# Performance work log

Hardware: AMD Instinct MI355X
Metric: run time of the kernel (lower is better)

Reference implementation:

```python
import jax, jax.numpy as jnp
import numpy as np

N, E, F_IN, D, B = 20000, 50000, 16, 64, 128


def setup_inputs() -> dict:
    key = jax.random.key(0)
    ks = jax.random.split(key, 24)
    s = 0.05
    inp = {
        "x": jax.random.normal(ks[0], (N, F_IN), jnp.float32),
        "edge_index": jax.random.randint(ks[1], (2, E), 0, N, jnp.int32),
        "edge_attr": jax.random.uniform(ks[2], (E, 5), jnp.float32),
        "batch": jnp.sort(jax.random.randint(ks[3], (N,), 0, B, jnp.int32)),
        # lin0
        "lin0_w": jax.random.normal(ks[4], (D, F_IN)) * s,
        "lin0_b": jnp.zeros((D,), jnp.float32),
        # edge MLP: Linear(5,128) -> ReLU -> Linear(128, D*D)
        "mlp_w1": jax.random.normal(ks[5], (128, 5)) * s,
        "mlp_b1": jnp.zeros((128,), jnp.float32),
        "mlp_w2": jax.random.normal(ks[6], (D * D, 128)) * s,
        "mlp_b2": jnp.zeros((D * D,), jnp.float32),
        # NNConv bias (root_weight=False, bias=True)
        "conv_b": jnp.zeros((D,), jnp.float32),
        # GRU(dim, dim), single layer
        "gru_w_ih": jax.random.normal(ks[7], (3 * D, D)) * s,
        "gru_w_hh": jax.random.normal(ks[8], (3 * D, D)) * s,
        "gru_b_ih": jnp.zeros((3 * D,), jnp.float32),
        "gru_b_hh": jnp.zeros((3 * D,), jnp.float32),
        # Set2Set LSTM(2*dim, dim)
        "lstm_w_ih": jax.random.normal(ks[9], (4 * D, 2 * D)) * s,
        "lstm_w_hh": jax.random.normal(ks[10], (4 * D, D)) * s,
        "lstm_b_ih": jnp.zeros((4 * D,), jnp.float32),
        "lstm_b_hh": jnp.zeros((4 * D,), jnp.float32),
    }
    return inp


def _gru_cell(x, h, w_ih, w_hh, b_ih, b_hh):
    gi = x @ w_ih.T + b_ih
    gh = h @ w_hh.T + b_hh
    i_r, i_z, i_n = jnp.split(gi, 3, axis=-1)
    h_r, h_z, h_n = jnp.split(gh, 3, axis=-1)
    r = jax.nn.sigmoid(i_r + h_r)
    z = jax.nn.sigmoid(i_z + h_z)
    n = jnp.tanh(i_n + r * h_n)
    return (1.0 - z) * n + z * h


def _lstm_cell(x, h, c, w_ih, w_hh, b_ih, b_hh):
    g = x @ w_ih.T + b_ih + h @ w_hh.T + b_hh
    i, f, gg, o = jnp.split(g, 4, axis=-1)
    c_new = jax.nn.sigmoid(f) * c + jax.nn.sigmoid(i) * jnp.tanh(gg)
    h_new = jax.nn.sigmoid(o) * jnp.tanh(c_new)
    return h_new, c_new


def reference(x, edge_index, edge_attr, batch,
              lin0_w, lin0_b, mlp_w1, mlp_b1, mlp_w2, mlp_b2, conv_b,
              gru_w_ih, gru_w_hh, gru_b_ih, gru_b_hh,
              lstm_w_ih, lstm_w_hh, lstm_b_ih, lstm_b_hh):
    src, dst = edge_index[0], edge_index[1]

    out = jax.nn.relu(x @ lin0_w.T + lin0_b)  # [N, D]
    h = out  # GRU hidden (seq_len=1 -> out == h after each step)

    # Edge-conditioned weights: MLP(edge_attr) -> [E, D, D]
    hidden = jax.nn.relu(edge_attr @ mlp_w1.T + mlp_b1)
    W_e = (hidden @ mlp_w2.T + mlp_b2).reshape(E, D, D)

    # in-degree counts for mean aggregation
    deg = jax.ops.segment_sum(jnp.ones((E,), x.dtype), dst, num_segments=N)
    deg = jnp.maximum(deg, 1.0)[:, None]

    for _ in range(3):
        # NNConv: gather src feats, per-edge matmul, scatter-mean to dst
        msg = jnp.einsum('ed,edo->eo', out[src], W_e)  # [E, D]
        agg = jax.ops.segment_sum(msg, dst, num_segments=N) / deg
        m = jax.nn.relu(agg + conv_b)
        h = _gru_cell(m, h, gru_w_ih, gru_w_hh, gru_b_ih, gru_b_hh)
        out = h

    # Set2Set pooling, 3 processing steps
    q_star = jnp.zeros((B, 2 * D), x.dtype)
    hh = jnp.zeros((B, D), x.dtype)
    cc = jnp.zeros((B, D), x.dtype)
    for _ in range(3):
        hh, cc = _lstm_cell(q_star, hh, cc, lstm_w_ih, lstm_w_hh, lstm_b_ih, lstm_b_hh)
        q = hh  # [B, D]
        e = jnp.sum(out * q[batch], axis=-1)  # [N]
        e_max = jax.ops.segment_max(e, batch, num_segments=B)
        a = jnp.exp(e - e_max[batch])
        a = a / jax.ops.segment_sum(a, batch, num_segments=B)[batch]
        r = jax.ops.segment_sum(a[:, None] * out, batch, num_segments=B)  # [B, D]
        q_star = jnp.concatenate([q, r], axis=-1)

    return q_star  # [B, 2*D]
```

## Files before the change

### kernel.cpp

```cpp
#include <hip/hip_runtime.h>
#include <hip/hip_bf16.h>

typedef float BF;
__device__ __forceinline__ float ldf(const BF* p, int i) { return p[i]; }

typedef _Float16 h8 __attribute__((ext_vector_type(8)));
typedef float f4 __attribute__((ext_vector_type(4)));

static constexpr int N_NODES = 20000;
static constexpr int N_EDGES = 50000;
static constexpr int E_PAD   = 50176;
static constexpr int N_MSGB  = 392;
static constexpr int N_PAD   = 20032;
static constexpr int BROW    = 136;
static constexpr int SROW    = 72;
static constexpr int N_B     = 79;
static constexpr int MAXSEG  = 2048;

__device__ __forceinline__ float sigf(float x) { return 1.f / (1.f + __expf(-x)); }
__device__ __forceinline__ float tanh_f(float x) {
  float e = __expf(2.f * x);
  return 1.f - 2.f / (e + 1.f);
}

static constexpr int S1_LIN0 = 5000;
static constexpr int S1_QS   = 2048;
static constexpr int S1_WCAT = 128;
static constexpr int S1_B2S  = 16;
static constexpr int S1_DEG  = 196;
static constexpr int PREP1_BLOCKS = S1_LIN0 + S1_QS + S1_WCAT + S1_B2S + 1 + 1 + S1_DEG;

__global__ void k_prep1(const BF* __restrict__ x, const int* __restrict__ batch,
                        const int* __restrict__ dst,
                        const BF* __restrict__ w0, const BF* __restrict__ b0,
                        const BF* __restrict__ w2, const BF* __restrict__ b2,
                        const BF* __restrict__ gwih, const BF* __restrict__ gwhh,
                        const BF* __restrict__ gbih, const BF* __restrict__ gbhh,
                        float* __restrict__ h, _Float16* __restrict__ h16,
                        _Float16* __restrict__ Qs, _Float16* __restrict__ Wcat,
                        float* __restrict__ bcat, _Float16* __restrict__ b2s,
                        int* __restrict__ seg, int* __restrict__ degi,
                        int* __restrict__ bsum) {
  int bid = blockIdx.x, t = threadIdx.x;
  if (bid < S1_LIN0) {
    __shared__ float xs[64];
    if (t < 64) xs[t] = ldf(x, bid * 64 + t);
    __syncthreads();
    int nl = t >> 6, o = t & 63;
    float acc = ldf(b0, o);
#pragma unroll
    for (int f = 0; f < 16; ++f) acc += xs[nl * 16 + f] * ldf(w0, o * 16 + f);
    float v = fmaxf(acc, 0.f);
    int idx = bid * 256 + t;
    h[idx] = v;
    h16[idx] = (_Float16)v;
    return;
  }
  bid -= S1_LIN0;
  if (bid < S1_QS) {
    int i = bid * 256 + t;
    int dl = i >> 13, rem = i & 8191;
    int f = rem >> 9, ln = (rem >> 3) & 63, j = i & 7;
    int o = (f & 3) * 16 + (ln & 15);
    int k = (f >> 2) * 32 + (ln >> 4) * 8 + j;
    Qs[i] = (_Float16)ldf(w2, (dl * 64 + o) * 128 + k);
    return;
  }
  bid -= S1_QS;
  if (bid < S1_WCAT) {
    int idx = bid * 256 + t, row = idx >> 7, k = idx & 127;
    int g = row >> 6, rr = row & 63;
    float v = 0.f;
    if (g == 0) v = (k < 64) ? ldf(gwih, rr * 64 + k) : ldf(gwhh, rr * 64 + (k - 64));
    else if (g == 1) v = (k < 64) ? ldf(gwih, (64 + rr) * 64 + k) : ldf(gwhh, (64 + rr) * 64 + (k - 64));
    else if (g == 2) v = (k < 64) ? ldf(gwih, (128 + rr) * 64 + k) : 0.f;
    else v = (k < 64) ? 0.f : ldf(gwhh, (128 + rr) * 64 + (k - 64));
    Wcat[idx] = (_Float16)v;
    return;
  }
  bid -= S1_WCAT;
  if (bid < S1_B2S) {
    int idx = bid * 256 + t;
    int f = idx >> 9, ln = (idx >> 3) & 63, j = idx & 7;
    int o = (f & 3) * 16 + (ln & 15);
    int d = (f >> 2) * 32 + (ln >> 4) * 8 + j;
    b2s[idx] = (_Float16)ldf(b2, d * 64 + o);
    return;
  }
  bid -= S1_B2S;
  if (bid == 0) {
    float v;
    if (t < 128) v = ldf(gbih, t) + ldf(gbhh, t);
    else if (t < 192) v = ldf(gbih, t);
    else v = ldf(gbhh, t - 64);
    bcat[t] = v;
    return;
  }
  bid -= 1;
  if (bid == 0) {
    if (t > 128) return;
    if (t == 128) { seg[128] = N_NODES; return; }
    int lo = 0, hi = N_NODES;
    while (lo < hi) {
      int mid = (lo + hi) >> 1;
      if (batch[mid] < t) lo = mid + 1; else hi = mid;
    }
    seg[t] = lo;
    return;
  }
  bid -= 1;
  {
    int e = bid * 256 + t;
    if (e < N_EDGES) {
      int d = dst[e];
      atomicAdd(&degi[d], 1);
      atomicAdd(&bsum[d >> 8], 1);
    }
  }
}

__global__ void k_scanA(const int* __restrict__ bsum, int* __restrict__ boff) {
  __shared__ int sd[128];
  int t = threadIdx.x;
  int x = (t < N_B) ? bsum[t] : 0;
  sd[t] = x;
  __syncthreads();
#pragma unroll
  for (int o = 1; o < 128; o <<= 1) {
    int val = (t >= o) ? sd[t - o] : 0;
    __syncthreads();
    sd[t] += val;
    __syncthreads();
  }
  if (t < N_B) boff[t] = sd[t] - x;
}

__global__ void k_scanB(const int* __restrict__ degi, const int* __restrict__ boff,
                        int* __restrict__ cursor) {
  __shared__ int sd[256];
  int b = blockIdx.x, t = threadIdx.x;
  int v = b * 256 + t;
  int x = (v < N_NODES) ? degi[v] : 0;
  sd[t] = x;
  __syncthreads();
#pragma unroll
  for (int o = 1; o < 256; o <<= 1) {
    int val = (t >= o) ? sd[t - o] : 0;
    __syncthreads();
    sd[t] += val;
    __syncthreads();
  }
  if (v < N_NODES) cursor[v] = boff[b] + sd[t] - x;
}

__global__ void k_fill(const int* __restrict__ dst, int* __restrict__ cursor,
                       int* __restrict__ eperm) {
  int e = blockIdx.x * 256 + threadIdx.x;
  if (e < N_EDGES) {
    int pos = atomicAdd(&cursor[dst[e]], 1);
    eperm[pos] = e;
  }
}

static constexpr int S2_MLP = E_PAD / 2;
static constexpr int S2_SP  = 196;

__global__ void k_prep2(const BF* __restrict__ ea, const int* __restrict__ src,
                        const int* __restrict__ dst, const int* __restrict__ eperm,
                        const BF* __restrict__ w1, const BF* __restrict__ b1,
                        _Float16* __restrict__ hidf, int* __restrict__ spadp,
                        int* __restrict__ dpadp) {
  int bid = blockIdx.x, t = threadIdx.x;
  if (bid < S2_MLP) {
    __shared__ float eas[10];
    __shared__ int el2[2];
    if (t < 2) { int pos = bid * 2 + t; el2[t] = (pos < N_EDGES) ? eperm[pos] : -1; }
    __syncthreads();
    if (t < 10) { int e = el2[t / 5]; eas[t] = (e >= 0) ? ldf(ea, e * 5 + (t % 5)) : 0.f; }
    __syncthreads();
    int le = t >> 7, j = t & 127;
    int pos = bid * 2 + le;
    float v = 0.f;
    if (pos < N_EDGES) {
      float acc = ldf(b1, j);
#pragma unroll
      for (int i = 0; i < 5; ++i) acc += eas[le * 5 + i] * ldf(w1, j * 5 + i);
      v = fmaxf(acc, 0.f);
    }
    hidf[(size_t)pos * 128 + j] = (_Float16)v;
    return;
  }
  bid -= S2_MLP;
  {
    int pos = bid * 256 + t;
    if (pos < E_PAD) {
      int e = (pos < N_EDGES) ? eperm[pos] : -1;
      spadp[pos] = (e >= 0) ? src[e] : 0;
      dpadp[pos] = (e >= 0) ? dst[e] : 0;
    }
  }
}

__launch_bounds__(256, 2)
__global__ void k_msg(const _Float16* __restrict__ h16, const _Float16* __restrict__ hidf,
                      const _Float16* __restrict__ Qs, const _Float16* __restrict__ b2s,
                      const int* __restrict__ spadp, const int* __restrict__ dpadp,
                      float* __restrict__ agg) {
  __shared__ _Float16 s_lds[128 * SROW];
  __shared__ _Float16 b_lds[2][8192];
  __shared__ _Float16 b2l[4096];
  const int tid = threadIdx.x;
  const int wv = tid >> 6, ln = tid & 63;
  const int m0 = ln & 15, quad = ln >> 4;
  const int tb = blockIdx.x * 128;

  {
    int el = tid >> 1, half = (tid & 1) * 32;
    int sp_ = spadp[tb + el];
    const uint4* hp4 = (const uint4*)(h16 + (size_t)sp_ * 64 + half);
    uint4 a0 = hp4[0], a1 = hp4[1], a2 = hp4[2], a3 = hp4[3];
    *(uint4*)&s_lds[el * SROW + half] = a0;
    *(uint4*)&s_lds[el * SROW + half + 8] = a1;
    *(uint4*)&s_lds[el * SROW + half + 16] = a2;
    *(uint4*)&s_lds[el * SROW + half + 24] = a3;
  }
  {
    const uint4* sp4 = (const uint4*)b2s;
    *(uint4*)&b2l[tid * 16] = sp4[tid * 2];
    *(uint4*)&b2l[tid * 16 + 8] = sp4[tid * 2 + 1];
  }
  h8 hvv[2][4];
#pragma unroll
  for (int mt = 0; mt < 2; ++mt) {
    int e = tb + wv * 32 + mt * 16 + m0;
    const _Float16* hp = hidf + (size_t)e * 128 + quad * 8;
#pragma unroll
    for (int c = 0; c < 4; ++c) hvv[mt][c] = *(const h8*)(hp + c * 32);
  }
  uint4 breg[4];
  {
    const uint4* qb = (const uint4*)Qs;
#pragma unroll
    for (int c = 0; c < 4; ++c) breg[c] = qb[tid + c * 256];
#pragma unroll
    for (int c = 0; c < 4; ++c) *(uint4*)&b_lds[0][(tid + c * 256) * 8] = breg[c];
  }
  __syncthreads();

  f4 acc[2][4];
#pragma unroll
  for (int mt = 0; mt < 2; ++mt)
#pragma unroll
    for (int ct = 0; ct < 4; ++ct)
#pragma unroll
      for (int j = 0; j < 4; ++j) acc[mt][ct][j] = 0.f;

  for (int dl = 0; dl < 64; ++dl) {
    int cur = dl & 1;
    if (dl < 63) {
      const uint4* qb = (const uint4*)(Qs + (size_t)(dl + 1) * 8192);
#pragma unroll
      for (int c = 0; c < 4; ++c) breg[c] = qb[tid + c * 256];
    }
    _Float16 sv0 = s_lds[(wv * 32 + m0) * SROW + dl];
    _Float16 sv1 = s_lds[(wv * 32 + 16 + m0) * SROW + dl];
#pragma unroll
    for (int t = 0; t < 4; ++t) {
      h8 a0 = hvv[0][t] * sv0;
      h8 a1 = hvv[1][t] * sv1;
#pragma unroll
      for (int ct = 0; ct < 4; ++ct) {
        h8 b = *(const h8*)&b_lds[cur][(t * 4 + ct) * 512 + ln * 8];
        acc[0][ct] = __builtin_amdgcn_mfma_f32_16x16x32_f16(a0, b, acc[0][ct], 0, 0, 0);
        acc[1][ct] = __builtin_amdgcn_mfma_f32_16x16x32_f16(a1, b, acc[1][ct], 0, 0, 0);
      }
    }
    if (dl < 63) {
#pragma unroll
      for (int c = 0; c < 4; ++c) *(uint4*)&b_lds[cur ^ 1][(tid + c * 256) * 8] = breg[c];
    }
    __syncthreads();
  }
#pragma unroll
  for (int tp = 0; tp < 2; ++tp) {
    h8 a0 = *(const h8*)&s_lds[(wv * 32 + m0) * SROW + tp * 32 + quad * 8];
    h8 a1 = *(const h8*)&s_lds[(wv * 32 + 16 + m0) * SROW + tp * 32 + quad * 8];
#pragma unroll
    for (int ct = 0; ct < 4; ++ct) {
      h8 b = *(const h8*)&b2l[(tp * 4 + ct) * 512 + ln * 8];
      acc[0][ct] = __builtin_amdgcn_mfma_f32_16x16x32_f16(a0, b, acc[0][ct], 0, 0, 0);
      acc[1][ct] = __builtin_amdgcn_mfma_f32_16x16x32_f16(a1, b, acc[1][ct], 0, 0, 0);
    }
  }
#pragma unroll
  for (int mt = 0; mt < 2; ++mt) {
#pragma unroll
    for (int r = 0; r < 4; ++r) {
      int pos = tb + wv * 32 + mt * 16 + quad * 4 + r;
      if (pos < N_EDGES) {
        float* ap = agg + (size_t)dpadp[pos] * 64 + m0;
#pragma unroll
        for (int ct = 0; ct < 4; ++ct) atomicAdd(ap + ct * 16, acc[mt][ct][r]);
      }
    }
  }
}

__launch_bounds__(256)
__global__ void k_gru(float* __restrict__ agg, const int* __restrict__ degi,
                      const BF* __restrict__ convb, const _Float16* __restrict__ W,
                      const float* __restrict__ bcat, float* __restrict__ h,
                      _Float16* __restrict__ h16) {
  __shared__ _Float16 xa[64 * BROW];
  __shared__ _Float16 wb[256 * BROW];
  __shared__ float bsh[256];
  int tid = threadIdx.x;
  int wv = tid >> 6, ln = tid & 63, m0 = ln & 15, quad = ln >> 4;
  int rowblk = blockIdx.x * 64;
  bsh[tid] = bcat[tid];
  {
    int r = tid >> 2, c0 = (tid & 3) * 16;
    int node = rowblk + r;
    _Float16 mv[16], hv[16];
    if (node < N_NODES) {
      float inv = 1.f / (float)max(degi[node], 1);
      float* ap = agg + (size_t)node * 64 + c0;
      const float* hp = h + (size_t)node * 64 + c0;
#pragma unroll
      for (int i = 0; i < 16; i += 4) {
        float4 a = *(float4*)(ap + i);
        *(float4*)(ap + i) = make_float4(0.f, 0.f, 0.f, 0.f);
        float4 hf = *(const float4*)(hp + i);
        mv[i + 0] = (_Float16)fmaxf(a.x * inv + ldf(convb, c0 + i + 0), 0.f);
        mv[i + 1] = (_Float16)fmaxf(a.y * inv + ldf(convb, c0 + i + 1), 0.f);
        mv[i + 2] = (_Float16)fmaxf(a.z * inv + ldf(convb, c0 + i + 2), 0.f);
        mv[i + 3] = (_Float16)fmaxf(a.w * inv + ldf(convb, c0 + i + 3), 0.f);
        hv[i + 0] = (_Float16)hf.x; hv[i + 1] = (_Float16)hf.y;
        hv[i + 2] = (_Float16)hf.z; hv[i + 3] = (_Float16)hf.w;
      }
    } else {
#pragma unroll
      for (int i = 0; i < 16; ++i) { mv[i] = (_Float16)0.f; hv[i] = (_Float16)0.f; }
    }
    *(uint4*)&xa[r * BROW + c0] = *(const uint4*)&mv[0];
    *(uint4*)&xa[r * BROW + c0 + 8] = *(const uint4*)&mv[8];
    *(uint4*)&xa[r * BROW + 64 + c0] = *(const uint4*)&hv[0];
    *(uint4*)&xa[r * BROW + 64 + c0 + 8] = *(const uint4*)&hv[8];
  }
#pragma unroll
  for (int c = 0; c < 16; ++c) {
    int i = tid + c * 256, r = i >> 4, ch = i & 15;
    *(uint4*)&wb[r * BROW + ch * 8] = *(const uint4*)(W + (size_t)r * 128 + ch * 8);
  }
  __syncthreads();
  f4 acc[16];
#pragma unroll
  for (int ct = 0; ct < 16; ++ct)
#pragma unroll
    for (int j = 0; j < 4; ++j) acc[ct][j] = 0.f;
#pragma unroll
  for (int t = 0; t < 4; ++t) {
    h8 a = *(const h8*)&xa[(wv * 16 + m0) * BROW + t * 32 + quad * 8];
#pragma unroll
    for (int ct = 0; ct < 16; ++ct) {
      h8 b = *(const h8*)&wb[(ct * 16 + m0) * BROW + t * 32 + quad * 8];
      acc[ct] = __builtin_amdgcn_mfma_f32_16x16x32_f16(a, b, acc[ct], 0, 0, 0);
    }
  }
#pragma unroll
  for (int c0 = 0; c0 < 4; ++c0) {
    int o = c0 * 16 + m0;
    float br = bsh[o], bz = bsh[64 + o], bn = bsh[128 + o], bh2 = bsh[192 + o];
#pragma unroll
    for (int r = 0; r < 4; ++r) {
      int row = rowblk + wv * 16 + quad * 4 + r;
      if (row < N_NODES) {
        float rr = sigf(acc[c0][r] + br);
        float zz = sigf(acc[c0 + 4][r] + bz);
        float nn = tanh_f(acc[c0 + 8][r] + bn + rr * (acc[c0 + 12][r] + bh2));
        size_t hi = (size_t)row * 64 + o;
        float hp = h[hi];
        float hn = (1.f - zz) * nn + zz * hp;
        h[hi] = hn;
        h16[hi] = (_Float16)hn;
      }
    }
  }
}

__launch_bounds__(1024)
__global__ void k_s2s(const float* __restrict__ h, const int* __restrict__ seg,
                      const BF* __restrict__ wih, const BF* __restrict__ whh,
                      const BF* __restrict__ bih, const BF* __restrict__ bhh,
                      float* __restrict__ outp) {
  __shared__ float xrow[128], g[256], qrow[64], hc[64], ccs[64], rr_[64];
  __shared__ float evals[MAXSEG];
  __shared__ float wred[16], wred2[16], rpart[16 * 64];
  int b = blockIdx.x, t = threadIdx.x;
  int wv = t >> 6, ln = t & 63;
  if (t < 64) { hc[t] = 0.f; ccs[t] = 0.f; rr_[t] = 0.f; }
  __syncthreads();
  int start = seg[b], end = seg[b + 1];
  int cnt = end - start;
  for (int st = 0; st < 3; ++st) {
    if (t < 64) xrow[t] = hc[t];
    else if (t < 128) xrow[t] = rr_[t - 64];
    __syncthreads();
    if (t < 256) {
      float acc = ldf(bih, t) + ldf(bhh, t);
      const float4* wr4 = (const float4*)(wih + t * 128);
#pragma unroll
      for (int i = 0; i < 32; ++i) {
        float4 wv4 = wr4[i];
        acc += xrow[i * 4] * wv4.x + xrow[i * 4 + 1] * wv4.y +
               xrow[i * 4 + 2] * wv4.z + xrow[i * 4 + 3] * wv4.w;
      }
      const float4* wr2 = (const float4*)(whh + t * 64);
#pragma unroll
      for (int i = 0; i < 16; ++i) {
        float4 wv4 = wr2[i];
        acc += xrow[i * 4] * wv4.x + xrow[i * 4 + 1] * wv4.y +
               xrow[i * 4 + 2] * wv4.z + xrow[i * 4 + 3] * wv4.w;
      }
      g[t] = acc;
    }
    __syncthreads();
    if (t < 64) {
      float ig = sigf(g[t]), fg = sigf(g[64 + t]);
      float gg = tanh_f(g[128 + t]), og = sigf(g[192 + t]);
      float c = fg * ccs[t] + ig * gg;
      ccs[t] = c;
      float hn = og * tanh_f(c);
      hc[t] = hn;
      qrow[t] = hn;
    }
    __syncthreads();
    float q = qrow[ln];
    float mw = -3.4e38f;
    for (int n0 = start + wv * 2; n0 < end; n0 += 32) {
      int n1 = n0 + 1;
      float p0 = h[(size_t)n0 * 64 + ln] * q;
      float p1 = (n1 < end) ? h[(size_t)n1 * 64 + ln] * q : 0.f;
#pragma unroll
      for (int off = 32; off > 0; off >>= 1) {
        p0 += __shfl_xor(p0, off);
        p1 += __shfl_xor(p1, off);
      }
      if (ln == 0) {
        evals[n0 - start] = p0;
        mw = fmaxf(mw, p0);
        if (n1 < end) { evals[n1 - start] = p1; mw = fmaxf(mw, p1); }
      }
    }
    if (ln == 0) wred[wv] = mw;
    __syncthreads();
    float gmax = -3.4e38f;
#pragma unroll
    for (int i = 0; i < 16; ++i) gmax = fmaxf(gmax, wred[i]);
    __syncthreads();
    float psum = 0.f;
    for (int i = t; i < cnt; i += 1024) {
      float a = __expf(evals[i] - gmax);
      evals[i] = a;
      psum += a;
    }
#pragma unroll
    for (int off = 32; off > 0; off >>= 1) psum += __shfl_xor(psum, off);
    if (ln == 0) wred2[wv] = psum;
    __syncthreads();
    float tsum = 0.f;
#pragma unroll
    for (int i = 0; i < 16; ++i) tsum += wred2[i];
    float inv = 1.f / fmaxf(tsum, 1e-30f);
    float racc = 0.f;
    for (int n0 = start + wv * 2; n0 < end; n0 += 32) {
      int n1 = n0 + 1;
      float a0 = evals[n0 - start] * h[(size_t)n0 * 64 + ln];
      float a1 = (n1 < end) ? evals[n1 - start] * h[(size_t)n1 * 64 + ln] : 0.f;
      racc += a0 + a1;
    }
    rpart[wv * 64 + ln] = racc;
    __syncthreads();
    if (t < 64) {
      float s = 0.f;
#pragma unroll
      for (int i = 0; i < 16; ++i) s += rpart[i * 64 + t];
      rr_[t] = s * inv;
    }
    __syncthreads();
  }
  if (t < 128) outp[b * 128 + t] = (t < 64) ? hc[t] : rr_[t - 64];
}

extern "C" void kernel_launch(void* const* d_in, const int* in_sizes, int n_in,
                              void* d_out, int out_size, void* d_ws, size_t ws_size,
                              hipStream_t stream) {
  const BF* x      = (const BF*)d_in[0];
  const int* ei    = (const int*)d_in[1];
  const BF* ea     = (const BF*)d_in[2];
  const int* batch = (const int*)d_in[3];
  const BF* w0     = (const BF*)d_in[4];
  const BF* b0     = (const BF*)d_in[5];
  const BF* w1     = (const BF*)d_in[6];
  const BF* b1     = (const BF*)d_in[7];
  const BF* w2     = (const BF*)d_in[8];
  const BF* b2     = (const BF*)d_in[9];
  const BF* convb  = (const BF*)d_in[10];
  const BF* gwih   = (const BF*)d_in[11];
  const BF* gwhh   = (const BF*)d_in[12];
  const BF* gbih   = (const BF*)d_in[13];
  const BF* gbhh   = (const BF*)d_in[14];
  const BF* lwih   = (const BF*)d_in[15];
  const BF* lwhh   = (const BF*)d_in[16];
  const BF* lbih   = (const BF*)d_in[17];
  const BF* lbhh   = (const BF*)d_in[18];
  const int* src = ei;
  const int* dstp = ei + N_EDGES;

  char* w = (char*)d_ws;
  size_t off_b = 0;
  auto take = [&](size_t bytes) -> void* {
    void* p = w + off_b;
    off_b = (off_b + bytes + 255) & ~(size_t)255;
    return p;
  };
  _Float16* Qs   = (_Float16*)take((size_t)4096 * 128 * 2);
  _Float16* hidf = (_Float16*)take((size_t)E_PAD * 128 * 2);
  float* h       = (float*)take((size_t)N_NODES * 64 * 4);
  _Float16* h16  = (_Float16*)take((size_t)N_NODES * 64 * 2);
  float* zr      = (float*)take((size_t)(N_NODES * 64 + N_NODES + 128) * 4);
  float* agg     = zr;
  int*   degi    = (int*)(zr + N_NODES * 64);
  int*   bsum    = degi + N_NODES;
  _Float16* Wcat = (_Float16*)take((size_t)256 * 128 * 2);
  float* bcat    = (float*)take((size_t)256 * 4);
  _Float16* b2s  = (_Float16*)take((size_t)8 * 512 * 2);
  int*   seg     = (int*)take((size_t)129 * 4);
  int*   boff    = (int*)take((size_t)128 * 4);
  int*   cursor  = (int*)take((size_t)N_NODES * 4);
  int*   eperm   = (int*)take((size_t)N_EDGES * 4);
  int*   spadp   = (int*)take((size_t)E_PAD * 4);
  int*   dpadp   = (int*)take((size_t)E_PAD * 4);

  hipMemsetAsync(zr, 0, (size_t)(N_NODES * 64 + N_NODES + 128) * 4, stream);
  k_prep1<<<PREP1_BLOCKS, 256, 0, stream>>>(x, batch, dstp, w0, b0, w2, b2,
                                            gwih, gwhh, gbih, gbhh,
                                            h, h16, Qs, Wcat, bcat, b2s,
                                            seg, degi, bsum);
  k_scanA<<<1, 128, 0, stream>>>(bsum, boff);
  k_scanB<<<N_B, 256, 0, stream>>>(degi, boff, cursor);
  k_fill<<<196, 256, 0, stream>>>(dstp, cursor, eperm);
  k_prep2<<<S2_MLP + S2_SP, 256, 0, stream>>>(ea, src, dstp, eperm, w1, b1,
                                              hidf, spadp, dpadp);
  for (int it = 0; it < 3; ++it) {
    k_msg<<<N_MSGB, 256, 0, stream>>>(h16, hidf, Qs, b2s, spadp, dpadp, agg);
    k_gru<<<N_PAD / 64, 256, 0, stream>>>(agg, degi, convb, Wcat, bcat, h, h16);
  }
  k_s2s<<<128, 1024, 0, stream>>>(h, seg, lwih, lwhh, lbih, lbhh, (float*)d_out);
}
```

Baseline: 467.5 us.

## Retile edge-message kernel to 256 edges by half output columns

The message kernel now processes 256 edges per block and splits the 64 output columns into two halves across a second grid dimension. The precomputed Qs weight layout is reordered to match. Each block streams half as much weight per step and reuses it across twice as many edges, with four M-tiles per wave. Separately, the edge-MLP prep now handles 8 edges per block instead of 2. The change raises register pressure from the larger accumulator and A-fragment sets, and the source-feature gather now loads a full 64-wide row per thread.

```diff
diff --git a/kernel.cpp b/kernel.cpp
--- a/kernel.cpp
+++ b/kernel.cpp
@@ -10,7 +10,7 @@
 static constexpr int N_NODES = 20000;
 static constexpr int N_EDGES = 50000;
 static constexpr int E_PAD   = 50176;
-static constexpr int N_MSGB  = 392;
+static constexpr int N_MSGB  = 196;
 static constexpr int N_PAD   = 20032;
 static constexpr int BROW    = 136;
 static constexpr int SROW    = 72;
@@ -59,10 +59,11 @@
   bid -= S1_LIN0;
   if (bid < S1_QS) {
     int i = bid * 256 + t;
-    int dl = i >> 13, rem = i & 8191;
-    int f = rem >> 9, ln = (rem >> 3) & 63, j = i & 7;
-    int o = (f & 3) * 16 + (ln & 15);
-    int k = (f >> 2) * 32 + (ln >> 4) * 8 + j;
+    int j = i & 7, ln = (i >> 3) & 63, f8 = (i >> 9) & 7;
+    int dl = (i >> 12) & 63, oh = i >> 18;
+    int tk = f8 >> 1, ctl = f8 & 1;
+    int o = oh * 32 + ctl * 16 + (ln & 15);
+    int k = tk * 32 + (ln >> 4) * 8 + j;
     Qs[i] = (_Float16)ldf(w2, (dl * 64 + o) * 128 + k);
     return;
   }
@@ -162,7 +163,7 @@
   }
 }
 
-static constexpr int S2_MLP = E_PAD / 2;
+static constexpr int S2_MLP = E_PAD / 8;
 static constexpr int S2_SP  = 196;
 
 __global__ void k_prep2(const BF* __restrict__ ea, const int* __restrict__ src,
@@ -172,22 +173,26 @@
                         int* __restrict__ dpadp) {
   int bid = blockIdx.x, t = threadIdx.x;
   if (bid < S2_MLP) {
-    __shared__ float eas[10];
-    __shared__ int el2[2];
-    if (t < 2) { int pos = bid * 2 + t; el2[t] = (pos < N_EDGES) ? eperm[pos] : -1; }
-    __syncthreads();
-    if (t < 10) { int e = el2[t / 5]; eas[t] = (e >= 0) ? ldf(ea, e * 5 + (t % 5)) : 0.f; }
-    __syncthreads();
-    int le = t >> 7, j = t & 127;
-    int pos = bid * 2 + le;
-    float v = 0.f;
-    if (pos < N_EDGES) {
-      float acc = ldf(b1, j);
-#pragma unroll
-      for (int i = 0; i < 5; ++i) acc += eas[le * 5 + i] * ldf(w1, j * 5 + i);
-      v = fmaxf(acc, 0.f);
-    }
-    hidf[(size_t)pos * 128 + j] = (_Float16)v;
+    __shared__ float eas[40];
+    __shared__ int el8[8];
+    if (t < 8) { int pos = bid * 8 + t; el8[t] = (pos < N_EDGES) ? eperm[pos] : -1; }
+    __syncthreads();
+    if (t < 40) { int e = el8[t / 5]; eas[t] = (e >= 0) ? ldf(ea, e * 5 + (t % 5)) : 0.f; }
+    __syncthreads();
+#pragma unroll
+    for (int rep = 0; rep < 4; ++rep) {
+      int item = t + rep * 256;
+      int le = item >> 7, j = item & 127;
+      int pos = bid * 8 + le;
+      float v = 0.f;
+      if (pos < N_EDGES) {
+        float acc = ldf(b1, j);
+#pragma unroll
+        for (int i = 0; i < 5; ++i) acc += eas[le * 5 + i] * ldf(w1, j * 5 + i);
+        v = fmaxf(acc, 0.f);
+      }
+      hidf[(size_t)pos * 128 + j] = (_Float16)v;
+    }
     return;
   }
   bid -= S2_MLP;
@@ -206,101 +211,106 @@
                       const _Float16* __restrict__ Qs, const _Float16* __restrict__ b2s,
                       const int* __restrict__ spadp, const int* __restrict__ dpadp,
                       float* __restrict__ agg) {
-  __shared__ _Float16 s_lds[128 * SROW];
-  __shared__ _Float16 b_lds[2][8192];
-  __shared__ _Float16 b2l[4096];
+  __shared__ _Float16 s_lds[256 * SROW];
+  __shared__ _Float16 b_lds[2][4096];
+  __shared__ _Float16 b2l[2048];
   const int tid = threadIdx.x;
   const int wv = tid >> 6, ln = tid & 63;
   const int m0 = ln & 15, quad = ln >> 4;
-  const int tb = blockIdx.x * 128;
+  const int tb = blockIdx.x * 256;
+  const int oh = blockIdx.y;
 
   {
-    int el = tid >> 1, half = (tid & 1) * 32;
-    int sp_ = spadp[tb + el];
-    const uint4* hp4 = (const uint4*)(h16 + (size_t)sp_ * 64 + half);
-    uint4 a0 = hp4[0], a1 = hp4[1], a2 = hp4[2], a3 = hp4[3];
-    *(uint4*)&s_lds[el * SROW + half] = a0;
-    *(uint4*)&s_lds[el * SROW + half + 8] = a1;
-    *(uint4*)&s_lds[el * SROW + half + 16] = a2;
-    *(uint4*)&s_lds[el * SROW + half + 24] = a3;
+    int sp_ = spadp[tb + tid];
+    const uint4* hp4 = (const uint4*)(h16 + (size_t)sp_ * 64);
+#pragma unroll
+    for (int c = 0; c < 8; ++c) *(uint4*)&s_lds[tid * SROW + c * 8] = hp4[c];
   }
   {
-    const uint4* sp4 = (const uint4*)b2s;
-    *(uint4*)&b2l[tid * 16] = sp4[tid * 2];
-    *(uint4*)&b2l[tid * 16 + 8] = sp4[tid * 2 + 1];
-  }
-  h8 hvv[2][4];
-#pragma unroll
-  for (int mt = 0; mt < 2; ++mt) {
-    int e = tb + wv * 32 + mt * 16 + m0;
+    int frag = tid >> 6, wi = tid & 63;
+    int tp = frag >> 1, ctl = frag & 1;
+    int sf = (tp << 2) | (oh * 2 + ctl);
+    *(uint4*)&b2l[frag * 512 + wi * 8] = *((const uint4*)b2s + sf * 64 + wi);
+  }
+  h8 hvv[4][4];
+#pragma unroll
+  for (int mt = 0; mt < 4; ++mt) {
+    int e = tb + wv * 64 + mt * 16 + m0;
     const _Float16* hp = hidf + (size_t)e * 128 + quad * 8;
 #pragma unroll
     for (int c = 0; c < 4; ++c) hvv[mt][c] = *(const h8*)(hp + c * 32);
   }
-  uint4 breg[4];
+  uint4 breg[2];
   {
-    const uint4* qb = (const uint4*)Qs;
-#pragma unroll
-    for (int c = 0; c < 4; ++c) breg[c] = qb[tid + c * 256];
-#pragma unroll
-    for (int c = 0; c < 4; ++c) *(uint4*)&b_lds[0][(tid + c * 256) * 8] = breg[c];
+    const uint4* qb = (const uint4*)(Qs + (size_t)(oh * 64) * 4096);
+    breg[0] = qb[tid];
+    breg[1] = qb[tid + 256];
+    *(uint4*)&b_lds[0][tid * 8] = breg[0];
+    *(uint4*)&b_lds[0][(tid + 256) * 8] = breg[1];
   }
   __syncthreads();
 
-  f4 acc[2][4];
-#pragma unroll
-  for (int mt = 0; mt < 2; ++mt)
-#pragma unroll
-    for (int ct = 0; ct < 4; ++ct)
+  f4 acc[4][2];
+#pragma unroll
+  for (int mt = 0; mt < 4; ++mt)
+#pragma unroll
+    for (int ct = 0; ct < 2; ++ct)
 #pragma unroll
       for (int j = 0; j < 4; ++j) acc[mt][ct][j] = 0.f;
 
   for (int dl = 0; dl < 64; ++dl) {
     int cur = dl & 1;
     if (dl < 63) {
-      const uint4* qb = (const uint4*)(Qs + (size_t)(dl + 1) * 8192);
-#pragma unroll
-      for (int c = 0; c < 4; ++c) breg[c] = qb[tid + c * 256];
-    }
-    _Float16 sv0 = s_lds[(wv * 32 + m0) * SROW + dl];
-    _Float16 sv1 = s_lds[(wv * 32 + 16 + m0) * SROW + dl];
-#pragma unroll
-    for (int t = 0; t < 4; ++t) {
-      h8 a0 = hvv[0][t] * sv0;
-      h8 a1 = hvv[1][t] * sv1;
-#pragma unroll
-      for (int ct = 0; ct < 4; ++ct) {
-        h8 b = *(const h8*)&b_lds[cur][(t * 4 + ct) * 512 + ln * 8];
-        acc[0][ct] = __builtin_amdgcn_mfma_f32_16x16x32_f16(a0, b, acc[0][ct], 0, 0, 0);
-        acc[1][ct] = __builtin_amdgcn_mfma_f32_16x16x32_f16(a1, b, acc[1][ct], 0, 0, 0);
+      const uint4* qb = (const uint4*)(Qs + (size_t)(oh * 64 + dl + 1) * 4096);
+      breg[0] = qb[tid];
+      breg[1] = qb[tid + 256];
+    }
+    _Float16 sv[4];
+#pragma unroll
+    for (int mt = 0; mt < 4; ++mt)
+      sv[mt] = s_lds[(wv * 64 + mt * 16 + m0) * SROW + dl];
+#pragma unroll
+    for (int tk = 0; tk < 4; ++tk) {
+      h8 a[4];
+#pragma unroll
+      for (int mt = 0; mt < 4; ++mt) a[mt] = hvv[mt][tk] * sv[mt];
+#pragma unroll
+      for (int ctl = 0; ctl < 2; ++ctl) {
+        h8 b = *(const h8*)&b_lds[cur][(tk * 2 + ctl) * 512 + ln * 8];
+#pragma unroll
+        for (int mt = 0; mt < 4; ++mt)
+          acc[mt][ctl] = __builtin_amdgcn_mfma_f32_16x16x32_f16(a[mt], b, acc[mt][ctl], 0, 0, 0);
       }
     }
     if (dl < 63) {
-#pragma unroll
-      for (int c = 0; c < 4; ++c) *(uint4*)&b_lds[cur ^ 1][(tid + c * 256) * 8] = breg[c];
+      *(uint4*)&b_lds[cur ^ 1][tid * 8] = breg[0];
+      *(uint4*)&b_lds[cur ^ 1][(tid + 256) * 8] = breg[1];
     }
     __syncthreads();
   }
 #pragma unroll
   for (int tp = 0; tp < 2; ++tp) {
-    h8 a0 = *(const h8*)&s_lds[(wv * 32 + m0) * SROW + tp * 32 + quad * 8];
-    h8 a1 = *(const h8*)&s_lds[(wv * 32 + 16 + m0) * SROW + tp * 32 + quad * 8];
-#pragma unroll
-    for (int ct = 0; ct < 4; ++ct) {
-      h8 b = *(const h8*)&b2l[(tp * 4 + ct) * 512 + ln * 8];
-      acc[0][ct] = __builtin_amdgcn_mfma_f32_16x16x32_f16(a0, b, acc[0][ct], 0, 0, 0);
-      acc[1][ct] = __builtin_amdgcn_mfma_f32_16x16x32_f16(a1, b, acc[1][ct], 0, 0, 0);
-    }
-  }
-#pragma unroll
-  for (int mt = 0; mt < 2; ++mt) {
+    h8 a[4];
+#pragma unroll
+    for (int mt = 0; mt < 4; ++mt)
+      a[mt] = *(const h8*)&s_lds[(wv * 64 + mt * 16 + m0) * SROW + tp * 32 + quad * 8];
+#pragma unroll
+    for (int ctl = 0; ctl < 2; ++ctl) {
+      h8 b = *(const h8*)&b2l[(tp * 2 + ctl) * 512 + ln * 8];
+#pragma unroll
+      for (int mt = 0; mt < 4; ++mt)
+        acc[mt][ctl] = __builtin_amdgcn_mfma_f32_16x16x32_f16(a[mt], b, acc[mt][ctl], 0, 0, 0);
+    }
+  }
+#pragma unroll
+  for (int mt = 0; mt < 4; ++mt) {
 #pragma unroll
     for (int r = 0; r < 4; ++r) {
-      int pos = tb + wv * 32 + mt * 16 + quad * 4 + r;
+      int pos = tb + wv * 64 + mt * 16 + quad * 4 + r;
       if (pos < N_EDGES) {
-        float* ap = agg + (size_t)dpadp[pos] * 64 + m0;
-#pragma unroll
-        for (int ct = 0; ct < 4; ++ct) atomicAdd(ap + ct * 16, acc[mt][ct][r]);
+        float* ap = agg + (size_t)dpadp[pos] * 64 + oh * 32 + m0;
+        atomicAdd(ap, acc[mt][0][r]);
+        atomicAdd(ap + 16, acc[mt][1][r]);
       }
     }
   }
@@ -553,7 +563,7 @@
   k_prep2<<<S2_MLP + S2_SP, 256, 0, stream>>>(ea, src, dstp, eperm, w1, b1,
                                               hidf, spadp, dpadp);
   for (int it = 0; it < 3; ++it) {
-    k_msg<<<N_MSGB, 256, 0, stream>>>(h16, hidf, Qs, b2s, spadp, dpadp, agg);
+    k_msg<<<dim3(N_MSGB, 2), 256, 0, stream>>>(h16, hidf, Qs, b2s, spadp, dpadp, agg);
     k_gru<<<N_PAD / 64, 256, 0, stream>>>(agg, degi, convb, Wcat, bcat, h, h16);
   }
   k_s2s<<<128, 1024, 0, stream>>>(h, seg, lwih, lwhh, lbih, lbhh, (float*)d_out);
```

New measurement: 443.5 us. 5.1% less time.
